# Optimization experiments

Measured on AMD Instinct MI355X. Metric: run time of the kernel, lower is better.

## Reference

```python
import jax, jax.numpy as jnp
from jax import lax
import numpy as np

EPS = 2.220446049250313e-16  # sys.float_info.epsilon


def setup_inputs() -> dict:
    key = jax.random.key(0)
    k1, k2, k3, k4 = jax.random.split(key, 4)
    C, H, W, R = 256, 256, 256, 16
    x = jax.random.normal(k1, (1, C, H, W), dtype=jnp.float32)
    w1 = jax.random.normal(k2, (R, C), dtype=jnp.float32) * 0.05   # Linear(C -> C//r), no bias
    w2 = jax.random.normal(k3, (C, R), dtype=jnp.float32) * 0.05   # Linear(C//r -> C), no bias
    conv_w = jax.random.normal(k4, (1, 2, 7, 7), dtype=jnp.float32) * 0.05  # Conv2d(2,1,7)
    return {"x": x, "w1": w1, "w2": w2, "conv_w": conv_w, "kv": 1}


def reference(x, w1, w2, conv_w, kv):
    b, c, h, w = x.shape  # b == 1 (module assumes batch 1 via squeeze(0))

    def fc(v):  # shared MLP of the channel attention
        return jnp.maximum(v @ w1.T, 0.0) @ w2.T

    y_avg = fc(x.mean(axis=(2, 3)))          # [1, C]
    y_max = fc(x.max(axis=(2, 3)))           # [1, C]
    y = jax.nn.sigmoid(y_avg + y_max)        # [1, C]

    yc = y[0]
    yc = (yc - yc.min()) / (yc.max() - yc.min() + 1e-20)  # min-max normalized gates in [0,1]

    # Batched SVD over channels replaces the per-channel Python loop.
    mats = x[0]                                            # [C, H, W]
    u, s, vh = jnp.linalg.svd(mats, full_matrices=False)   # u:[C,H,K] s:[C,K] vh:[C,K,W]
    K = s.shape[-1]
    # k = int(len(s) * kv * yc[c]); singular values are sorted descending, so
    # top-k selection == keep the first k -> mask the tail.
    k = jnp.floor(K * kv * yc).astype(jnp.int32)           # [C]
    keep = jnp.arange(K)[None, :] < k[:, None]             # [C, K]
    s_m = jnp.where(keep, s, 0.0)
    recon = jnp.einsum('chk,ck,ckw->chw', u, s_m, vh)      # low-rank reconstruction
    x2 = recon[None]                                       # [1, C, H, W]

    avg_out = x2.mean(axis=1, keepdims=True)
    max_out = x2.max(axis=1, keepdims=True)
    cat = jnp.concatenate([avg_out, max_out], axis=1)      # [1, 2, H, W]
    out = lax.conv_general_dilated(cat, conv_w, (1, 1), [(3, 3), (3, 3)],
                                   dimension_numbers=('NCHW', 'OIHW', 'NCHW'))
    out = jnp.where(out < EPS, EPS, out)
    return jax.nn.sigmoid(out)
```

## Files before the change

### kernel.cpp

```cpp
#include <hip/hip_runtime.h>


#define NCH 256
#define N 256
#define NN 65536
#define NS_MAX 22

#define OFF_K 0
#define OFF_MODE 256
#define OFF_MC 512
#define OFF_COEF 768
#define OFF_SUM 12032
#define OFF_MAXHW 77568
#define OFF_MEAND 143104
#define OFF_MAXD 143616
#define OFF_T 144128
#define OFF_ALPHA 144640
#define OFF_AQ 145152
#define OFF_BQ 276224
#define OFF_ITSW 407296
#define SMALL_FLOATS 407552

#define NSH_LDS 135168
#define F16_PANEL 33792

static const float EPSF = 2.220446049250313e-16f;

typedef unsigned short u16;
typedef _Float16 h8 __attribute__((ext_vector_type(8)));
typedef float f32x4 __attribute__((ext_vector_type(4)));

__device__ __forceinline__ float rdlane(float v, int l) {
  return __uint_as_float(__builtin_amdgcn_readlane(__float_as_uint(v), l));
}

__device__ __forceinline__ u16 f2h(float v) {
  _Float16 h = (_Float16)v;
  u16 u;
  __builtin_memcpy(&u, &h, 2);
  return u;
}
__device__ __forceinline__ float h2f(u16 u) {
  _Float16 h;
  __builtin_memcpy(&h, &u, 2);
  return (float)h;
}

__device__ __forceinline__ double block_sum1024d(double v, double* red, int tid) {
  for (int off = 32; off; off >>= 1) v += __shfl_down(v, off, 64);
  __syncthreads();
  if ((tid & 63) == 0) red[tid >> 6] = v;
  __syncthreads();
  double s = 0.0;
#pragma unroll
  for (int i = 0; i < 16; ++i) s += red[i];
  return s;
}

__global__ __launch_bounds__(256) void k_chan_stats(const float* __restrict__ x,
                                                    float* __restrict__ small) {
  int c = blockIdx.x, tid = threadIdx.x;
  const float4* xc = (const float4*)(x + (size_t)c * NN);
  double s = 0.0;
  float m = -1e30f;
  for (int i = tid; i < NN / 4; i += 256) {
    float4 v = xc[i];
    s += (double)v.x + (double)v.y + (double)v.z + (double)v.w;
    m = fmaxf(m, fmaxf(fmaxf(v.x, v.y), fmaxf(v.z, v.w)));
  }
  __shared__ double rs[4];
  __shared__ float rm[4];
  for (int off = 32; off; off >>= 1) {
    s += __shfl_down(s, off, 64);
    m = fmaxf(m, __shfl_down(m, off, 64));
  }
  if ((tid & 63) == 0) { rs[tid >> 6] = s; rm[tid >> 6] = m; }
  __syncthreads();
  if (tid == 0) {
    ((double*)(small + OFF_MEAND))[c] = (rs[0] + rs[1] + rs[2] + rs[3]) / (double)NN;
    ((double*)(small + OFF_MAXD))[c] =
        (double)fmaxf(fmaxf(rm[0], rm[1]), fmaxf(rm[2], rm[3]));
  }
}

__global__ __launch_bounds__(256) void k_attention(const float* __restrict__ w1,
                                                   const float* __restrict__ w2,
                                                   const int* __restrict__ kvp,
                                                   float* __restrict__ small) {
  int tid = threadIdx.x;
  __shared__ double ha[16], hm[16], redd[8], ymn[256], ymx[256];
  double va = ((const double*)(small + OFF_MEAND))[tid];
  double vm = ((const double*)(small + OFF_MAXD))[tid];
  for (int r = 0; r < 16; ++r) {
    double wv = (double)w1[r * 256 + tid];
    double pa = wv * va, pm = wv * vm;
    for (int off = 32; off; off >>= 1) {
      pa += __shfl_down(pa, off, 64);
      pm += __shfl_down(pm, off, 64);
    }
    if ((tid & 63) == 0) { redd[tid >> 6] = pa; redd[4 + (tid >> 6)] = pm; }
    __syncthreads();
    if (tid == 0) {
      ha[r] = fmax(redd[0] + redd[1] + redd[2] + redd[3], 0.0);
      hm[r] = fmax(redd[4] + redd[5] + redd[6] + redd[7], 0.0);
    }
    __syncthreads();
  }
  double ya = 0.0, ym = 0.0;
  for (int r = 0; r < 16; ++r) {
    double wv = (double)w2[tid * 16 + r];
    ya += ha[r] * wv;
    ym += hm[r] * wv;
  }
  double y = 1.0 / (1.0 + exp(-(ya + ym)));
  ymn[tid] = y; ymx[tid] = y;
  __syncthreads();
  for (int off = 128; off; off >>= 1) {
    if (tid < off) {
      ymn[tid] = fmin(ymn[tid], ymn[tid + off]);
      ymx[tid] = fmax(ymx[tid], ymx[tid + off]);
    }
    __syncthreads();
  }
  double yc = (y - ymn[0]) / (ymx[0] - ymn[0] + 1e-20);
  int kv = kvp[0];
  int k = (int)floor(256.0 * (double)kv * yc);
  int mode = (k <= 0) ? 0 : ((k >= 256) ? 1 : 2);
  int* ip = (int*)small;
  ip[OFF_K + tid] = k;
  ip[OFF_MODE + tid] = mode;
}

#define GEMM128_VARS                                                           \
  int tid = threadIdx.x;                                                       \
  int tx4 = (tid & 15) * 4, ty4 = (tid >> 4) * 4;                              \
  int lm = tid >> 1, lq = (tid & 1) * 2;                                       \
  int lk = tid >> 4, lc = (tid & 15) * 2;                                      \
  (void)lk; (void)lc;

#define STORE_T128(Ls, v0, v1)                                                 \
  Ls[lq * 4 + 0][lm] = v0.x; Ls[lq * 4 + 1][lm] = v0.y;                        \
  Ls[lq * 4 + 2][lm] = v0.z; Ls[lq * 4 + 3][lm] = v0.w;                        \
  Ls[lq * 4 + 4][lm] = v1.x; Ls[lq * 4 + 5][lm] = v1.y;                        \
  Ls[lq * 4 + 6][lm] = v1.z; Ls[lq * 4 + 7][lm] = v1.w;

#define GEMM128_INNER(AsM, BsM)                                                \
  _Pragma("unroll") for (int kk = 0; kk < 16; ++kk) {                          \
    float4 a0 = *(const float4*)&AsM[kk][ty4];                                 \
    float4 a1 = *(const float4*)&AsM[kk][64 + ty4];                            \
    float4 b0 = *(const float4*)&BsM[kk][tx4];                                 \
    float4 b1 = *(const float4*)&BsM[kk][64 + tx4];                            \
    float av[8] = {a0.x, a0.y, a0.z, a0.w, a1.x, a1.y, a1.z, a1.w};            \
    float bv[8] = {b0.x, b0.y, b0.z, b0.w, b1.x, b1.y, b1.z, b1.w};            \
    _Pragma("unroll") for (int rr = 0; rr < 8; ++rr)                           \
      _Pragma("unroll") for (int cc2 = 0; cc2 < 8; ++cc2)                      \
        acc[rr][cc2] += av[rr] * bv[cc2];                                      \
  }

#define WRITE_TILE_NORM(Cc)                                                    \
  _Pragma("unroll") for (int rh = 0; rh < 2; ++rh)                             \
  _Pragma("unroll") for (int rr = 0; rr < 4; ++rr) {                           \
    int rI = rh * 4 + rr;                                                      \
    float* rowp = (Cc) + (size_t)(i0 + rh * 64 + ty4 + rr) * N + j0;           \
    *(float4*)(rowp + tx4) =                                                   \
        make_float4(acc[rI][0], acc[rI][1], acc[rI][2], acc[rI][3]);           \
    *(float4*)(rowp + 64 + tx4) =                                              \
        make_float4(acc[rI][4], acc[rI][5], acc[rI][6], acc[rI][7]);           \
  }

#define WRITE_TILE_MIRROR(Cc)                                                  \
  _Pragma("unroll") for (int ch = 0; ch < 2; ++ch)                             \
  _Pragma("unroll") for (int cc2 = 0; cc2 < 4; ++cc2) {                        \
    int cI = ch * 4 + cc2;                                                     \
    float* rowp = (Cc) + (size_t)(j0 + ch * 64 + tx4 + cc2) * N + i0;          \
    *(float4*)(rowp + ty4) =                                                   \
        make_float4(acc[0][cI], acc[1][cI], acc[2][cI], acc[3][cI]);           \
    *(float4*)(rowp + 64 + ty4) =                                              \
        make_float4(acc[4][cI], acc[5][cI], acc[6][cI], acc[7][cI]);           \
  }

#define SYM_MAP                                                                \
  int bx = blockIdx.x;                                                         \
  int i0 = (bx >= 1) ? 128 : 0, j0 = (bx == 2) ? 128 : 0;

__global__ __launch_bounds__(256) void k_gram(const float* __restrict__ x,
                                              float* __restrict__ bufA, int base) {
  __shared__ float As[16][132], Bs[16][132];
  GEMM128_VARS; SYM_MAP;
  const float* A = x + (size_t)(base + blockIdx.z) * NN;
  float acc[8][8] = {};
  const float* Ap = A + (size_t)(i0 + lm) * N + lq * 4;
  const float* Bp = A + (size_t)(j0 + lm) * N + lq * 4;
  float4 va0 = *(const float4*)Ap, va1 = *(const float4*)(Ap + 4);
  float4 vb0 = *(const float4*)Bp, vb1 = *(const float4*)(Bp + 4);
  for (int kt = 0; kt < 16; ++kt) {
    __syncthreads();
    STORE_T128(As, va0, va1); STORE_T128(Bs, vb0, vb1);
    __syncthreads();
    if (kt < 15) {
      va0 = *(const float4*)(Ap + (kt + 1) * 16);
      va1 = *(const float4*)(Ap + (kt + 1) * 16 + 4);
      vb0 = *(const float4*)(Bp + (kt + 1) * 16);
      vb1 = *(const float4*)(Bp + (kt + 1) * 16 + 4);
    }
    GEMM128_INNER(As, Bs);
  }
  float* Cc = bufA + (size_t)blockIdx.z * NN;
  WRITE_TILE_NORM(Cc);
  if (bx == 1) { WRITE_TILE_MIRROR(Cc); }
}

__global__ __launch_bounds__(1024) void k_tridiag(const float* __restrict__ Gall,
                                                  float* __restrict__ small, int base) {
  extern __shared__ double dls[];
  double* redd = dls;
  double* pip = dls + 16;
  float* P = (float*)(dls + 1040);
  float* uf = P + 32896;
  float* wf = uf + 256;
  int tid = threadIdx.x, lane = tid & 63;
  int r = tid & 255, g = tid >> 8;
  int R0 = ((tid >> 6) & 3) << 6;
  int c = base + blockIdx.x;
  const int* ip = (const int*)small;
  if (ip[OFF_MODE + c] != 2) return;
  const float* G = Gall + (size_t)blockIdx.x * NN;
  double* aq = (double*)(small + OFF_AQ) + (size_t)c * 256;
  double* bq = (double*)(small + OFF_BQ) + (size_t)c * 256;
  const int triR = (r * (r + 1)) >> 1;

  for (int i = g; i < N; i += 4)
    if (r <= i) P[((i * (i + 1)) >> 1) + r] = G[i * N + r];
  __syncthreads();

  for (int j = 0; j + 2 < N; ++j) {
    if (g == 0 && r >= j + 1) uf[r] = P[triR + j];
    __syncthreads();
    float ur0 = uf[r];
    double part = (g == 0 && r >= j + 2) ? (double)ur0 * (double)ur0 : 0.0;
    double x0 = (double)uf[j + 1];
    double sigma = block_sum1024d(part, redd, tid);
    if (sigma <= 1e-40) {
      if (tid == 0) bq[j] = x0;
      __syncthreads();
      continue;
    }
    double nu = sqrt(x0 * x0 + sigma);
    double bsub = (x0 >= 0.0) ? -nu : nu;
    double beta = 1.0 / (nu * (nu + fabs(x0)));
    if (tid == j + 1) uf[tid] = (float)(x0 - bsub);
    __syncthreads();
    int cbase = (j + 1) & ~63;
    int c0 = cbase + 64 * g;
    float ureg = 0.f;
    if (c0 < N) ureg = uf[c0 + lane];
    double myp = 0.0;
    if (c0 < N) {
      int lbeg = (c0 > j + 1) ? c0 : (j + 1);
      int lend = c0 + 64;
      if (lbeg < lend) {
        double pi0 = 0.0, pi1 = 0.0, pi2 = 0.0, pi3 = 0.0;
        if (c0 + 64 <= R0) {
          int lmv = lbeg;
          for (; lmv + 3 < lend; lmv += 4) {
            float uv0 = rdlane(ureg, lmv - c0), uv1 = rdlane(ureg, lmv + 1 - c0);
            float uv2 = rdlane(ureg, lmv + 2 - c0), uv3 = rdlane(ureg, lmv + 3 - c0);
            float v0 = P[triR + lmv], v1 = P[triR + lmv + 1];
            float v2 = P[triR + lmv + 2], v3 = P[triR + lmv + 3];
            pi0 += (double)v0 * (double)uv0;
            pi1 += (double)v1 * (double)uv1;
            pi2 += (double)v2 * (double)uv2;
            pi3 += (double)v3 * (double)uv3;
          }
          for (; lmv < lend; ++lmv)
            pi0 += (double)P[triR + lmv] * (double)rdlane(ureg, lmv - c0);
        } else if (c0 >= R0 + 64) {
          int lmv = lbeg;
          int s = (lmv * (lmv + 1)) >> 1;
          for (; lmv + 3 < lend; lmv += 4) {
            int s0 = s, s1 = s0 + lmv + 1, s2 = s1 + lmv + 2, s3 = s2 + lmv + 3;
            s = s3 + lmv + 4;
            float uv0 = rdlane(ureg, lmv - c0), uv1 = rdlane(ureg, lmv + 1 - c0);
            float uv2 = rdlane(ureg, lmv + 2 - c0), uv3 = rdlane(ureg, lmv + 3 - c0);
            pi0 += (double)P[s0 + r] * (double)uv0;
            pi1 += (double)P[s1 + r] * (double)uv1;
            pi2 += (double)P[s2 + r] * (double)uv2;
            pi3 += (double)P[s3 + r] * (double)uv3;
          }
          for (; lmv < lend; ++lmv) {
            pi0 += (double)P[s + r] * (double)rdlane(ureg, lmv - c0);
            s += lmv + 1;
          }
        } else {
          int lmv = lbeg;
          int s = (lmv * (lmv + 1)) >> 1;
          for (; lmv < lend; ++lmv) {
            float uv = rdlane(ureg, lmv - c0);
            float v = P[(lmv <= r) ? (triR + lmv) : (s + r)];
            pi0 += (double)v * (double)uv;
            s += lmv + 1;
          }
        }
        myp = (pi0 + pi1) + (pi2 + pi3);
      }
    }
    pip[tid] = (r >= j + 1) ? myp : 0.0;
    __syncthreads();
    double ur = (r >= j + 1) ? (double)uf[r] : 0.0;
    double pi = 0.0;
    if (g == 0 && r >= j + 1)
      pi = (pip[r] + pip[256 + r] + pip[512 + r] + pip[768 + r]) * beta;
    double kpart = (g == 0) ? ur * pi : 0.0;
    double K = block_sum1024d(kpart, redd, tid) * beta * 0.5;
    if (g == 0) wf[r] = (float)(pi - K * ur);
    __syncthreads();
    float wreg = 0.f;
    if (c0 < N) wreg = wf[c0 + lane];
    if (c0 < N && r >= j + 1) {
      float urf = uf[r];
      float wrf = wf[r];
      int lbeg = (c0 > j + 1) ? c0 : (j + 1);
      int lend = c0 + 64;
      int lcap = (r | 63) + 1;
      if (lend > lcap) lend = lcap;
      if (c0 + 64 <= R0) {
        int lmv = lbeg;
        for (; lmv + 1 < lend; lmv += 2) {
          float uv0 = rdlane(ureg, lmv - c0), wv0 = rdlane(wreg, lmv - c0);
          float uv1 = rdlane(ureg, lmv + 1 - c0), wv1 = rdlane(wreg, lmv + 1 - c0);
          P[triR + lmv] = fmaf(-wrf, uv0, fmaf(-urf, wv0, P[triR + lmv]));
          P[triR + lmv + 1] = fmaf(-wrf, uv1, fmaf(-urf, wv1, P[triR + lmv + 1]));
        }
        if (lmv < lend) {
          float uv0 = rdlane(ureg, lmv - c0), wv0 = rdlane(wreg, lmv - c0);
          P[triR + lmv] = fmaf(-wrf, uv0, fmaf(-urf, wv0, P[triR + lmv]));
        }
      } else if (c0 == R0) {
        for (int lmv = lbeg; lmv < lend; ++lmv) {
          float uv = rdlane(ureg, lmv - c0), wv = rdlane(wreg, lmv - c0);
          if (lmv <= r)
            P[triR + lmv] = fmaf(-wrf, uv, fmaf(-urf, wv, P[triR + lmv]));
        }
      }
    }
    if (tid == 0) bq[j] = bsub;
    __syncthreads();
  }
  if (g == 0) aq[r] = (double)P[triR + r];
  if (tid == 0) bq[N - 2] = (double)P[(((N - 1) * N) >> 1) + N - 2];
}

__device__ __forceinline__ int sturm_count_lds(const double* a, const double* b,
                                               double t) {
  double d = a[0] - t;
  int cnt = (d < 0.0);
  for (int i = 1; i < N; ++i) {
    double den = d;
    if (fabs(den) < 1e-20) den = (den < 0.0) ? -1e-20 : 1e-20;
    double bb = b[i - 1];
    d = (a[i] - t) - bb * bb / den;
    cnt += (d < 0.0);
  }
  return cnt;
}

__global__ __launch_bounds__(64) void k_bisect(float* __restrict__ small,
                                               int base, int cc) {
  int ci = blockIdx.x;
  if (ci >= cc) return;
  int c = base + ci, lane = threadIdx.x;
  int* ip = (int*)small;
  if (ip[OFF_MODE + c] != 2) {
    if (lane == 0) { ip[OFF_MC + c] = 0; ip[OFF_ITSW + c] = 0; }
    return;
  }
  int k = ip[OFF_K + c];
  const double* a = (const double*)(small + OFF_AQ) + (size_t)c * 256;
  const double* b = (const double*)(small + OFF_BQ) + (size_t)c * 256;
  __shared__ double sa[256], sb[256];
  for (int i = lane; i < N; i += 64) {
    sa[i] = a[i];
    if (i < N - 1) sb[i] = b[i];
  }
  __syncthreads();
  double lo = 1e300, hi = -1e300;
  for (int i = lane; i < N; i += 64) {
    double rr = (i > 0 ? fabs(sb[i - 1]) : 0.0) + (i < N - 1 ? fabs(sb[i]) : 0.0);
    lo = fmin(lo, sa[i] - rr);
    hi = fmax(hi, sa[i] + rr);
  }
  for (int off = 32; off; off >>= 1) {
    lo = fmin(lo, __shfl_xor(lo, off, 64));
    hi = fmax(hi, __shfl_xor(hi, off, 64));
  }
  double lamk = 0.0, lamk1 = 0.0;
  for (int which = 0; which < 2; ++which) {
    int j = (which == 0) ? (N - k + 1) : (N - k);
    double l0 = lo, h0 = hi;
    for (int pass = 0; pass < 10; ++pass) {
      double step = (h0 - l0) * (1.0 / 65.0);
      double t = l0 + step * (double)(lane + 1);
      int cnt = sturm_count_lds(sa, sb, t);
      unsigned long long mask = __ballot(cnt >= j);
      if (mask == 0ull) {
        l0 = l0 + step * 64.0;
      } else {
        int bpos = __ffsll((long long)mask) - 1;
        double nl = (bpos == 0) ? l0 : (l0 + step * (double)bpos);
        h0 = l0 + step * (double)(bpos + 1);
        l0 = nl;
      }
    }
    double v = 0.5 * (l0 + h0);
    if (which == 0) lamk = v; else lamk1 = v;
  }
  if (lane == 0) {
    double t = 0.5 * (lamk + lamk1);
    double gap = fmax(lamk - lamk1, 0.0);
    double alpha = 1.002 * fmax(hi - t, t - lo) + 1e-30;
    double g0 = fmax(gap / (2.0 * alpha), 2e-6);
    float* cf = small + OFF_COEF + (size_t)c * (2 * NS_MAX);
    double l = fmin(g0, 0.99);
    int m = 0, isw = NS_MAX;
    while (m < NS_MAX - 2 && l < 0.9999) {
      if (isw == NS_MAX && l >= 0.02) isw = m;
      double aa = sqrt(27.0 / (4.0 * (1.0 + l + l * l)));
      double bb = (4.0 / 27.0) * aa * aa * aa;
      cf[2 * m] = (float)aa;
      cf[2 * m + 1] = (float)bb;
      double pl = aa * l - bb * l * l * l;
      double p1 = aa - bb;
      l = fmin(pl, p1);
      m++;
    }
    for (int e = 0; e < 2; ++e) {
      if (isw == NS_MAX && l >= 0.02) isw = m;
      cf[2 * m] = 1.5f; cf[2 * m + 1] = 0.5f; m++;
    }
    if (isw > m) isw = m;
    ip[OFF_MC + c] = m;
    ip[OFF_ITSW + c] = isw;
    ((double*)(small + OFF_T))[c] = t;
    ((double*)(small + OFF_ALPHA))[c] = alpha;
  }
}

__global__ void k_x0(const float* __restrict__ small, float* __restrict__ bufA,
                     int base) {
  int ci = blockIdx.y, c = base + ci;
  const int* ip = (const int*)small;
  if (ip[OFF_MODE + c] != 2) return;
  double t = ((const double*)(small + OFF_T))[c];
  double inva = 1.0 / ((const double*)(small + OFF_ALPHA))[c];
  float* X = bufA + (size_t)ci * NN;
  int r = blockIdx.x, tid = threadIdx.x;
  double gg = (double)X[r * N + tid];
  if (tid == r) gg -= t;
  X[r * N + tid] = (float)(gg * inva);
}

__global__ __launch_bounds__(256) void k_ns1(const float* __restrict__ src,
                                             float* __restrict__ Sb,
                                             const float* __restrict__ small,
                                             int base, int it) {
  const int* ip = (const int*)small;
  int c = base + blockIdx.z;
  if (ip[OFF_MODE + c] != 2 || it >= ip[OFF_ITSW + c]) return;
  __shared__ float As[16][132], Bs[16][132];
  GEMM128_VARS; SYM_MAP;
  const float* X = src + (size_t)blockIdx.z * NN;
  float acc[8][8] = {};
  const float* Ap = X + (size_t)(i0 + lm) * N + lq * 4;
  const float* Bp = X + (size_t)(j0 + lm) * N + lq * 4;
  float4 va0 = *(const float4*)Ap, va1 = *(const float4*)(Ap + 4);
  float4 vb0 = *(const float4*)Bp, vb1 = *(const float4*)(Bp + 4);
  for (int kt = 0; kt < 16; ++kt) {
    __syncthreads();
    STORE_T128(As, va0, va1); STORE_T128(Bs, vb0, vb1);
    __syncthreads();
    if (kt < 15) {
      va0 = *(const float4*)(Ap + (kt + 1) * 16);
      va1 = *(const float4*)(Ap + (kt + 1) * 16 + 4);
      vb0 = *(const float4*)(Bp + (kt + 1) * 16);
      vb1 = *(const float4*)(Bp + (kt + 1) * 16 + 4);
    }
    GEMM128_INNER(As, Bs);
  }
  float* Cc = Sb + (size_t)blockIdx.z * NN;
  WRITE_TILE_NORM(Cc);
  if (bx == 1) { WRITE_TILE_MIRROR(Cc); }
}

__global__ __launch_bounds__(256) void k_ns2(const float* __restrict__ src,
                                             const float* __restrict__ Sb,
                                             float* __restrict__ dst,
                                             const float* __restrict__ small,
                                             int base, int it) {
  const int* ip = (const int*)small;
  int c = base + blockIdx.z;
  if (ip[OFF_MODE + c] != 2 || it >= ip[OFF_ITSW + c]) return;
  float ca = small[OFF_COEF + (size_t)c * (2 * NS_MAX) + 2 * it];
  float cb = small[OFF_COEF + (size_t)c * (2 * NS_MAX) + 2 * it + 1];
  __shared__ float As[16][132], Bs[16][132];
  GEMM128_VARS; SYM_MAP;
  const float* X = src + (size_t)blockIdx.z * NN;
  const float* S = Sb + (size_t)blockIdx.z * NN;
  float acc[8][8] = {};
  const float* Ap = X + (size_t)(i0 + lm) * N + lq * 4;
  const float* Bp = S + (size_t)(j0 + lm) * N + lq * 4;
  float4 va0 = *(const float4*)Ap, va1 = *(const float4*)(Ap + 4);
  float4 vb0 = *(const float4*)Bp, vb1 = *(const float4*)(Bp + 4);
  for (int kt = 0; kt < 16; ++kt) {
    __syncthreads();
    STORE_T128(As, va0, va1); STORE_T128(Bs, vb0, vb1);
    __syncthreads();
    if (kt < 15) {
      va0 = *(const float4*)(Ap + (kt + 1) * 16);
      va1 = *(const float4*)(Ap + (kt + 1) * 16 + 4);
      vb0 = *(const float4*)(Bp + (kt + 1) * 16);
      vb1 = *(const float4*)(Bp + (kt + 1) * 16 + 4);
    }
    GEMM128_INNER(As, Bs);
  }
#pragma unroll
  for (int rh = 0; rh < 2; ++rh)
#pragma unroll
    for (int rr = 0; rr < 4; ++rr) {
      int rI = rh * 4 + rr;
      const float* rowp = X + (size_t)(i0 + rh * 64 + ty4 + rr) * N + j0;
      float4 x0 = *(const float4*)(rowp + tx4);
      float4 x1 = *(const float4*)(rowp + 64 + tx4);
      acc[rI][0] = ca * x0.x - cb * acc[rI][0];
      acc[rI][1] = ca * x0.y - cb * acc[rI][1];
      acc[rI][2] = ca * x0.z - cb * acc[rI][2];
      acc[rI][3] = ca * x0.w - cb * acc[rI][3];
      acc[rI][4] = ca * x1.x - cb * acc[rI][4];
      acc[rI][5] = ca * x1.y - cb * acc[rI][5];
      acc[rI][6] = ca * x1.z - cb * acc[rI][6];
      acc[rI][7] = ca * x1.w - cb * acc[rI][7];
    }
  float* Y = dst + (size_t)blockIdx.z * NN;
  WRITE_TILE_NORM(Y);
  if (bx == 1) { WRITE_TILE_MIRROR(Y); }
}

__device__ __forceinline__ void stage_h(u16* pan, const u16* g16, int tid) {
#pragma unroll
  for (int i = 0; i < 16; ++i) {
    int g = tid * 16 + i * 4096;
    int lo = g + ((g >> 9) << 4);
    *(uint4*)((char*)pan + lo) = *(const uint4*)((const char*)g16 + g);
  }
}
__device__ __forceinline__ void stage_f(u16* pan, const float* gF, int tid) {
#pragma unroll
  for (int i = 0; i < 16; ++i) {
    int e = tid * 8 + i * 2048;
    float4 v0 = *(const float4*)(gF + e);
    float4 v1 = *(const float4*)(gF + e + 4);
    h8 hv;
    hv[0] = (_Float16)v0.x; hv[1] = (_Float16)v0.y;
    hv[2] = (_Float16)v0.z; hv[3] = (_Float16)v0.w;
    hv[4] = (_Float16)v1.x; hv[5] = (_Float16)v1.y;
    hv[6] = (_Float16)v1.z; hv[7] = (_Float16)v1.w;
    int b = e * 2;
    int lo = b + ((b >> 9) << 4);
    *(h8*)((char*)pan + lo) = hv;
  }
}

__global__ __launch_bounds__(256) void k_nsh(const float* __restrict__ srcF,
                                             float* __restrict__ Sf,
                                             float* __restrict__ dstF,
                                             const float* __restrict__ small,
                                             int base, int it, int phase) {
  const int* ip = (const int*)small;
  int ci = blockIdx.z, c = base + ci;
  if (ip[OFF_MODE + c] != 2) return;
  int isw = ip[OFF_ITSW + c], mc = ip[OFF_MC + c];
  if (it < isw || it >= mc) return;
  SYM_MAP;
  extern __shared__ char ldsraw[];
  u16* Apan = (u16*)ldsraw;
  u16* Bpan = Apan + F16_PANEL;
  int tid = threadIdx.x;
  bool cvtA = (it == isw);
  bool sameP = (phase == 0) && (bx != 1);
  const float* XF = srcF + (size_t)ci * NN;
  const u16* XH = (const u16*)XF;
  if (cvtA) stage_f(Apan, XF + (size_t)i0 * N, tid);
  else      stage_h(Apan, XH + (size_t)i0 * N, tid);
  if (!sameP) {
    if (phase == 0) {
      if (cvtA) stage_f(Bpan, XF + (size_t)j0 * N, tid);
      else      stage_h(Bpan, XH + (size_t)j0 * N, tid);
    } else {
      const u16* SH = (const u16*)(Sf + (size_t)ci * NN);
      stage_h(Bpan, SH + (size_t)j0 * N, tid);
    }
  }
  const u16* Bb = sameP ? Apan : Bpan;
  __syncthreads();

  int l = tid & 63, wid = tid >> 6;
  int wr = (wid >> 1) * 64, wc = (wid & 1) * 64;
  int rA = wr + (l & 15), rB = wc + (l & 15);
  int kB = (l >> 4) << 3;
  f32x4 zero = {0.f, 0.f, 0.f, 0.f};
  f32x4 acc[4][4];
#pragma unroll
  for (int mi = 0; mi < 4; ++mi)
#pragma unroll
    for (int ni = 0; ni < 4; ++ni) acc[mi][ni] = zero;

#pragma unroll
  for (int kc = 0; kc < 8; ++kc) {
    int kof = kc * 32 + kB;
    h8 af[4], bf[4];
#pragma unroll
    for (int mi = 0; mi < 4; ++mi)
      af[mi] = *(const h8*)((const char*)Apan +
                            ((size_t)(rA + mi * 16) * 264 + kof) * 2);
#pragma unroll
    for (int ni = 0; ni < 4; ++ni)
      bf[ni] = *(const h8*)((const char*)Bb +
                            ((size_t)(rB + ni * 16) * 264 + kof) * 2);
#pragma unroll
    for (int mi = 0; mi < 4; ++mi)
#pragma unroll
      for (int ni = 0; ni < 4; ++ni)
        acc[mi][ni] = __builtin_amdgcn_mfma_f32_16x16x32_f16(
            af[mi], bf[ni], acc[mi][ni], 0, 0, 0);
  }

  float cav = 0.f, cbv = 0.f;
  bool last = false;
  if (phase) {
    cav = small[OFF_COEF + (size_t)c * (2 * NS_MAX) + 2 * it];
    cbv = small[OFF_COEF + (size_t)c * (2 * NS_MAX) + 2 * it + 1];
    last = (it == mc - 1);
  }
  float* oF = dstF + (size_t)ci * NN;
  u16* oH = phase ? (u16*)oF : (u16*)(Sf + (size_t)ci * NN);
  int lr4 = (l >> 4) << 2, lcn = l & 15;
#pragma unroll
  for (int mi = 0; mi < 4; ++mi)
#pragma unroll
    for (int ni = 0; ni < 4; ++ni)
#pragma unroll
      for (int rg = 0; rg < 4; ++rg) {
        int gr = i0 + wr + mi * 16 + lr4 + rg;
        int gc = j0 + wc + ni * 16 + lcn;
        float v = acc[mi][ni][rg];
        if (phase) {
          float xv = h2f(Apan[(size_t)(gr - i0) * 264 + gc]);
          v = cav * xv - cbv * v;
        }
        if (!last) {
          u16 hv = f2h(v);
          oH[(size_t)gr * N + gc] = hv;
          if (bx == 1) oH[(size_t)gc * N + gr] = hv;
        } else {
          oF[(size_t)gr * N + gc] = v;
          if (bx == 1) oF[(size_t)gc * N + gr] = v;
        }
      }
}

__global__ __launch_bounds__(256) void k_proj(const float* __restrict__ bufA,
                                              const float* __restrict__ bufB,
                                              const float* __restrict__ x,
                                              float* __restrict__ bufC,
                                              const float* __restrict__ small,
                                              int base) {
  const int* ip = (const int*)small;
  int ci = blockIdx.z, c = base + ci;
  int mode = ip[OFF_MODE + c];
  GEMM128_VARS;
  int i0 = blockIdx.x * 128, j0 = blockIdx.y * 128;
  float* Cc = bufC + (size_t)ci * NN;
  const float* xc = x + (size_t)c * NN;
  if (mode != 2) {
#pragma unroll
    for (int rh = 0; rh < 2; ++rh)
#pragma unroll
      for (int rr = 0; rr < 4; ++rr) {
        size_t ro = (size_t)(i0 + rh * 64 + ty4 + rr) * N + j0;
        if (mode == 0) {
          *(float4*)(Cc + ro + tx4) = make_float4(0.f, 0.f, 0.f, 0.f);
          *(float4*)(Cc + ro + 64 + tx4) = make_float4(0.f, 0.f, 0.f, 0.f);
        } else {
          *(float4*)(Cc + ro + tx4) = *(const float4*)(xc + ro + tx4);
          *(float4*)(Cc + ro + 64 + tx4) = *(const float4*)(xc + ro + 64 + tx4);
        }
      }
    return;
  }
  int mc = ip[OFF_MC + c];
  const float* Xh = ((mc & 1) ? bufB : bufA) + (size_t)ci * NN;
  __shared__ float As[16][132], Bs[16][132];
  float acc[8][8] = {};
  const float* Ap = Xh + (size_t)(i0 + lm) * N + lq * 4;
  const float* Bp = xc + (size_t)lk * N + j0 + lc * 4;
  float4 va0 = *(const float4*)Ap, va1 = *(const float4*)(Ap + 4);
  float4 vb0 = *(const float4*)Bp, vb1 = *(const float4*)(Bp + 4);
  for (int kt = 0; kt < 16; ++kt) {
    __syncthreads();
    STORE_T128(As, va0, va1);
    *(float4*)&Bs[lk][lc * 4] = vb0;
    *(float4*)&Bs[lk][(lc + 1) * 4] = vb1;
    __syncthreads();
    if (kt < 15) {
      va0 = *(const float4*)(Ap + (kt + 1) * 16);
      va1 = *(const float4*)(Ap + (kt + 1) * 16 + 4);
      const float* Bp2 = xc + (size_t)((kt + 1) * 16 + lk) * N + j0 + lc * 4;
      vb0 = *(const float4*)Bp2;
      vb1 = *(const float4*)(Bp2 + 4);
    }
    GEMM128_INNER(As, Bs);
  }
#pragma unroll
  for (int rh = 0; rh < 2; ++rh)
#pragma unroll
    for (int rr = 0; rr < 4; ++rr) {
      int rI = rh * 4 + rr;
      const float* rowp = xc + (size_t)(i0 + rh * 64 + ty4 + rr) * N + j0;
      float4 x0 = *(const float4*)(rowp + tx4);
      float4 x1 = *(const float4*)(rowp + 64 + tx4);
      acc[rI][0] = 0.5f * (acc[rI][0] + x0.x);
      acc[rI][1] = 0.5f * (acc[rI][1] + x0.y);
      acc[rI][2] = 0.5f * (acc[rI][2] + x0.z);
      acc[rI][3] = 0.5f * (acc[rI][3] + x0.w);
      acc[rI][4] = 0.5f * (acc[rI][4] + x1.x);
      acc[rI][5] = 0.5f * (acc[rI][5] + x1.y);
      acc[rI][6] = 0.5f * (acc[rI][6] + x1.z);
      acc[rI][7] = 0.5f * (acc[rI][7] + x1.w);
    }
  WRITE_TILE_NORM(Cc);
}

__global__ void k_accum(const float* __restrict__ bufC, float* __restrict__ sum_hw,
                        float* __restrict__ max_hw, int cc, int first) {
  int p = blockIdx.x * 256 + threadIdx.x;
  float s = first ? 0.f : sum_hw[p];
  float m = first ? -1e30f : max_hw[p];
  for (int ci = 0; ci < cc; ++ci) {
    float v = bufC[(size_t)ci * NN + p];
    s += v;
    m = fmaxf(m, v);
  }
  sum_hw[p] = s;
  max_hw[p] = m;
}

__global__ void k_conv(const float* __restrict__ sum_hw, const float* __restrict__ max_hw,
                       const float* __restrict__ cw, float* __restrict__ out) {
  int p = blockIdx.x * 256 + threadIdx.x;
  int h = p >> 8, w = p & 255;
  float acc = 0.f;
  for (int dy = 0; dy < 7; ++dy) {
    int hy = h + dy - 3;
    if (hy < 0 || hy > 255) continue;
    for (int dx = 0; dx < 7; ++dx) {
      int wx = w + dx - 3;
      if (wx < 0 || wx > 255) continue;
      int q = hy * 256 + wx;
      acc += cw[dy * 7 + dx] * (sum_hw[q] * (1.f / 256.f)) +
             cw[49 + dy * 7 + dx] * max_hw[q];
    }
  }
  acc = fmaxf(acc, EPSF);
  out[p] = 1.f / (1.f + expf(-acc));
}

extern "C" void kernel_launch(void* const* d_in, const int* in_sizes, int n_in,
                              void* d_out, int out_size, void* d_ws, size_t ws_size,
                              hipStream_t stream) {
  const float* x = (const float*)d_in[0];
  const float* w1 = (const float*)d_in[1];
  const float* w2 = (const float*)d_in[2];
  const float* cw = (const float*)d_in[3];
  const int* kv = (const int*)d_in[4];
  float* out = (float*)d_out;
  float* small = (float*)d_ws;

  size_t small_bytes = (size_t)SMALL_FLOATS * 4;
  size_t avail = ws_size > small_bytes ? ws_size - small_bytes : 0;
  long chunk = (long)(avail / (3ull * NN * 4));
  if (chunk > NCH) chunk = NCH;
  if (chunk < 1) chunk = 1;
  float* bufA = small + SMALL_FLOATS;
  float* bufB = bufA + (size_t)chunk * NN;
  float* bufC = bufB + (size_t)chunk * NN;

  const int tridiag_lds = 1040 * 8 + 32896 * 4 + 512 * 4;
  hipFuncSetAttribute((const void*)k_tridiag,
                      hipFuncAttributeMaxDynamicSharedMemorySize, tridiag_lds);
  hipFuncSetAttribute((const void*)k_nsh,
                      hipFuncAttributeMaxDynamicSharedMemorySize, NSH_LDS);

  k_chan_stats<<<NCH, 256, 0, stream>>>(x, small);
  k_attention<<<1, 256, 0, stream>>>(w1, w2, kv, small);

  const int IT32 = 13;

  for (int base = 0; base < NCH; base += (int)chunk) {
    int cc = (NCH - base < (int)chunk) ? (NCH - base) : (int)chunk;
    dim3 gsym(3, 1, cc);
    dim3 gproj(2, 2, cc);
    k_gram<<<gsym, 256, 0, stream>>>(x, bufA, base);
    k_tridiag<<<cc, 1024, tridiag_lds, stream>>>(bufA, small, base);
    k_bisect<<<cc, 64, 0, stream>>>(small, base, cc);
    k_x0<<<dim3(N, cc), 256, 0, stream>>>(small, bufA, base);
    for (int it = 0; it < NS_MAX; ++it) {
      const float* src = (it & 1) ? bufB : bufA;
      float* dst = (it & 1) ? bufA : bufB;
      if (it < IT32) {
        k_ns1<<<gsym, 256, 0, stream>>>(src, bufC, small, base, it);
        k_ns2<<<gsym, 256, 0, stream>>>(src, bufC, dst, small, base, it);
      }
      k_nsh<<<gsym, 256, NSH_LDS, stream>>>(src, bufC, dst, small, base, it, 0);
      k_nsh<<<gsym, 256, NSH_LDS, stream>>>(src, bufC, dst, small, base, it, 1);
    }
    k_proj<<<gproj, 256, 0, stream>>>(bufA, bufB, x, bufC, small, base);
    k_accum<<<256, 256, 0, stream>>>(bufC, small + OFF_SUM, small + OFF_MAXHW, cc,
                                     base == 0 ? 1 : 0);
  }
  k_conv<<<256, 256, 0, stream>>>(small + OFF_SUM, small + OFF_MAXHW, cw, out);
}
```

Measured before the change: 5.786 ms.

## Restructure tridiagonalization to 512 threads and fold norm and matvec into one barrier phase

The Householder tridiagonalization kernel now runs with 512 threads, so each wave handles two 64-column chunks instead of one. The sigma reduction is overlapped with the symmetric matvec: the matvec is computed with the un-modified Householder vector, and the pivot-element change is corrected afterwards with a rank-one fix term. This removes roughly two block barriers per column step and replaces the generic 16-entry block reduction with an 8-wave one. The cost is fewer threads doing the matvec and update work, and a small numerical difference from the corrected-pivot formulation.

```diff
diff --git a/kernel.cpp b/kernel.cpp
--- a/kernel.cpp
+++ b/kernel.cpp
@@ -46,17 +46,6 @@
   return (float)h;
 }
 
-__device__ __forceinline__ double block_sum1024d(double v, double* red, int tid) {
-  for (int off = 32; off; off >>= 1) v += __shfl_down(v, off, 64);
-  __syncthreads();
-  if ((tid & 63) == 0) red[tid >> 6] = v;
-  __syncthreads();
-  double s = 0.0;
-#pragma unroll
-  for (int i = 0; i < 16; ++i) s += red[i];
-  return s;
-}
-
 __global__ __launch_bounds__(256) void k_chan_stats(const float* __restrict__ x,
                                                     float* __restrict__ small) {
   int c = blockIdx.x, tid = threadIdx.x;
@@ -210,17 +199,102 @@
   if (bx == 1) { WRITE_TILE_MIRROR(Cc); }
 }
 
-__global__ __launch_bounds__(1024) void k_tridiag(const float* __restrict__ Gall,
-                                                  float* __restrict__ small, int base) {
+__device__ __forceinline__ double mv_chunk(const float* __restrict__ P, int c0,
+                                           int j, int r, int R0, int triR,
+                                           float ureg) {
+  double pi0 = 0.0, pi1 = 0.0, pi2 = 0.0, pi3 = 0.0;
+  if (c0 < N) {
+    int lbeg = (c0 > j + 1) ? c0 : (j + 1);
+    int lend = c0 + 64;
+    if (lbeg < lend) {
+      if (c0 + 64 <= R0) {
+        int lmv = lbeg;
+        for (; lmv + 3 < lend; lmv += 4) {
+          float uv0 = rdlane(ureg, lmv - c0), uv1 = rdlane(ureg, lmv + 1 - c0);
+          float uv2 = rdlane(ureg, lmv + 2 - c0), uv3 = rdlane(ureg, lmv + 3 - c0);
+          float v0 = P[triR + lmv], v1 = P[triR + lmv + 1];
+          float v2 = P[triR + lmv + 2], v3 = P[triR + lmv + 3];
+          pi0 += (double)v0 * (double)uv0;
+          pi1 += (double)v1 * (double)uv1;
+          pi2 += (double)v2 * (double)uv2;
+          pi3 += (double)v3 * (double)uv3;
+        }
+        for (; lmv < lend; ++lmv)
+          pi0 += (double)P[triR + lmv] * (double)rdlane(ureg, lmv - c0);
+      } else if (c0 >= R0 + 64) {
+        int lmv = lbeg;
+        int s = (lmv * (lmv + 1)) >> 1;
+        for (; lmv + 3 < lend; lmv += 4) {
+          int s0 = s, s1 = s0 + lmv + 1, s2 = s1 + lmv + 2, s3 = s2 + lmv + 3;
+          s = s3 + lmv + 4;
+          float uv0 = rdlane(ureg, lmv - c0), uv1 = rdlane(ureg, lmv + 1 - c0);
+          float uv2 = rdlane(ureg, lmv + 2 - c0), uv3 = rdlane(ureg, lmv + 3 - c0);
+          pi0 += (double)P[s0 + r] * (double)uv0;
+          pi1 += (double)P[s1 + r] * (double)uv1;
+          pi2 += (double)P[s2 + r] * (double)uv2;
+          pi3 += (double)P[s3 + r] * (double)uv3;
+        }
+        for (; lmv < lend; ++lmv) {
+          pi0 += (double)P[s + r] * (double)rdlane(ureg, lmv - c0);
+          s += lmv + 1;
+        }
+      } else {
+        int lmv = lbeg;
+        int s = (lmv * (lmv + 1)) >> 1;
+        for (; lmv < lend; ++lmv) {
+          float uv = rdlane(ureg, lmv - c0);
+          float v = P[(lmv <= r) ? (triR + lmv) : (s + r)];
+          pi0 += (double)v * (double)uv;
+          s += lmv + 1;
+        }
+      }
+    }
+  }
+  return (pi0 + pi1) + (pi2 + pi3);
+}
+
+__device__ __forceinline__ void upd_chunk(float* __restrict__ P, int c0, int j,
+                                          int r, int R0, int triR, float ureg,
+                                          float wreg, float urf, float wrf) {
+  if (c0 >= N) return;
+  int lbeg = (c0 > j + 1) ? c0 : (j + 1);
+  int lend = c0 + 64;
+  int lcap = (r | 63) + 1;
+  if (lend > lcap) lend = lcap;
+  if (c0 + 64 <= R0) {
+    int lmv = lbeg;
+    for (; lmv + 1 < lend; lmv += 2) {
+      float uv0 = rdlane(ureg, lmv - c0), wv0 = rdlane(wreg, lmv - c0);
+      float uv1 = rdlane(ureg, lmv + 1 - c0), wv1 = rdlane(wreg, lmv + 1 - c0);
+      P[triR + lmv] = fmaf(-wrf, uv0, fmaf(-urf, wv0, P[triR + lmv]));
+      P[triR + lmv + 1] = fmaf(-wrf, uv1, fmaf(-urf, wv1, P[triR + lmv + 1]));
+    }
+    if (lmv < lend) {
+      float uv0 = rdlane(ureg, lmv - c0), wv0 = rdlane(wreg, lmv - c0);
+      P[triR + lmv] = fmaf(-wrf, uv0, fmaf(-urf, wv0, P[triR + lmv]));
+    }
+  } else if (c0 == R0) {
+    for (int lmv = lbeg; lmv < lend; ++lmv) {
+      float uv = rdlane(ureg, lmv - c0), wv = rdlane(wreg, lmv - c0);
+      if (lmv <= r)
+        P[triR + lmv] = fmaf(-wrf, uv, fmaf(-urf, wv, P[triR + lmv]));
+    }
+  }
+}
+
+__global__ __launch_bounds__(512) void k_tridiag(const float* __restrict__ Gall,
+                                                 float* __restrict__ small, int base) {
   extern __shared__ double dls[];
   double* redd = dls;
+  double* redd2 = dls + 8;
   double* pip = dls + 16;
-  float* P = (float*)(dls + 1040);
+  float* P = (float*)(dls + 528);
   float* uf = P + 32896;
   float* wf = uf + 256;
   int tid = threadIdx.x, lane = tid & 63;
   int r = tid & 255, g = tid >> 8;
-  int R0 = ((tid >> 6) & 3) << 6;
+  int wid = tid >> 6;
+  int R0 = (wid & 3) << 6;
   int c = base + blockIdx.x;
   const int* ip = (const int*)small;
   if (ip[OFF_MODE + c] != 2) return;
@@ -229,119 +303,63 @@
   double* bq = (double*)(small + OFF_BQ) + (size_t)c * 256;
   const int triR = (r * (r + 1)) >> 1;
 
-  for (int i = g; i < N; i += 4)
+  for (int i = g; i < N; i += 2)
     if (r <= i) P[((i * (i + 1)) >> 1) + r] = G[i * N + r];
   __syncthreads();
 
   for (int j = 0; j + 2 < N; ++j) {
     if (g == 0 && r >= j + 1) uf[r] = P[triR + j];
     __syncthreads();
-    float ur0 = uf[r];
-    double part = (g == 0 && r >= j + 2) ? (double)ur0 * (double)ur0 : 0.0;
+    float x_r = uf[r];
     double x0 = (double)uf[j + 1];
-    double sigma = block_sum1024d(part, redd, tid);
+    int cbase = (j + 1) & ~63;
+    int c0a = cbase + 128 * g, c0b = c0a + 64;
+    float urega = 0.f, uregb = 0.f;
+    if (c0a < N) urega = uf[c0a + lane];
+    if (c0b < N) uregb = uf[c0b + lane];
+    double sp = (g == 0 && r >= j + 2) ? (double)x_r * (double)x_r : 0.0;
+    double myp = mv_chunk(P, c0a, j, r, R0, triR, urega) +
+                 mv_chunk(P, c0b, j, r, R0, triR, uregb);
+    pip[tid] = (r >= j + 1) ? myp : 0.0;
+    for (int off = 32; off; off >>= 1) sp += __shfl_down(sp, off, 64);
+    if (lane == 0) redd[wid] = sp;
+    __syncthreads();
+    double sigma = ((redd[0] + redd[1]) + (redd[2] + redd[3])) +
+                   ((redd[4] + redd[5]) + (redd[6] + redd[7]));
     if (sigma <= 1e-40) {
       if (tid == 0) bq[j] = x0;
-      __syncthreads();
       continue;
     }
     double nu = sqrt(x0 * x0 + sigma);
     double bsub = (x0 >= 0.0) ? -nu : nu;
     double beta = 1.0 / (nu * (nu + fabs(x0)));
-    if (tid == j + 1) uf[tid] = (float)(x0 - bsub);
-    __syncthreads();
-    int cbase = (j + 1) & ~63;
-    int c0 = cbase + 64 * g;
-    float ureg = 0.f;
-    if (c0 < N) ureg = uf[c0 + lane];
-    double myp = 0.0;
-    if (c0 < N) {
-      int lbeg = (c0 > j + 1) ? c0 : (j + 1);
-      int lend = c0 + 64;
-      if (lbeg < lend) {
-        double pi0 = 0.0, pi1 = 0.0, pi2 = 0.0, pi3 = 0.0;
-        if (c0 + 64 <= R0) {
-          int lmv = lbeg;
-          for (; lmv + 3 < lend; lmv += 4) {
-            float uv0 = rdlane(ureg, lmv - c0), uv1 = rdlane(ureg, lmv + 1 - c0);
-            float uv2 = rdlane(ureg, lmv + 2 - c0), uv3 = rdlane(ureg, lmv + 3 - c0);
-            float v0 = P[triR + lmv], v1 = P[triR + lmv + 1];
-            float v2 = P[triR + lmv + 2], v3 = P[triR + lmv + 3];
-            pi0 += (double)v0 * (double)uv0;
-            pi1 += (double)v1 * (double)uv1;
-            pi2 += (double)v2 * (double)uv2;
-            pi3 += (double)v3 * (double)uv3;
-          }
-          for (; lmv < lend; ++lmv)
-            pi0 += (double)P[triR + lmv] * (double)rdlane(ureg, lmv - c0);
-        } else if (c0 >= R0 + 64) {
-          int lmv = lbeg;
-          int s = (lmv * (lmv + 1)) >> 1;
-          for (; lmv + 3 < lend; lmv += 4) {
-            int s0 = s, s1 = s0 + lmv + 1, s2 = s1 + lmv + 2, s3 = s2 + lmv + 3;
-            s = s3 + lmv + 4;
-            float uv0 = rdlane(ureg, lmv - c0), uv1 = rdlane(ureg, lmv + 1 - c0);
-            float uv2 = rdlane(ureg, lmv + 2 - c0), uv3 = rdlane(ureg, lmv + 3 - c0);
-            pi0 += (double)P[s0 + r] * (double)uv0;
-            pi1 += (double)P[s1 + r] * (double)uv1;
-            pi2 += (double)P[s2 + r] * (double)uv2;
-            pi3 += (double)P[s3 + r] * (double)uv3;
-          }
-          for (; lmv < lend; ++lmv) {
-            pi0 += (double)P[s + r] * (double)rdlane(ureg, lmv - c0);
-            s += lmv + 1;
-          }
-        } else {
-          int lmv = lbeg;
-          int s = (lmv * (lmv + 1)) >> 1;
-          for (; lmv < lend; ++lmv) {
-            float uv = rdlane(ureg, lmv - c0);
-            float v = P[(lmv <= r) ? (triR + lmv) : (s + r)];
-            pi0 += (double)v * (double)uv;
-            s += lmv + 1;
-          }
-        }
-        myp = (pi0 + pi1) + (pi2 + pi3);
-      }
-    }
-    pip[tid] = (r >= j + 1) ? myp : 0.0;
-    __syncthreads();
-    double ur = (r >= j + 1) ? (double)uf[r] : 0.0;
-    double pi = 0.0;
-    if (g == 0 && r >= j + 1)
-      pi = (pip[r] + pip[256 + r] + pip[512 + r] + pip[768 + r]) * beta;
-    double kpart = (g == 0) ? ur * pi : 0.0;
-    double K = block_sum1024d(kpart, redd, tid) * beta * 0.5;
-    if (g == 0) wf[r] = (float)(pi - K * ur);
-    __syncthreads();
-    float wreg = 0.f;
-    if (c0 < N) wreg = wf[c0 + lane];
-    if (c0 < N && r >= j + 1) {
-      float urf = uf[r];
+    if (c0a <= j + 1 && j + 1 < c0a + 64 && lane == j + 1 - c0a)
+      urega = (float)(x0 - bsub);
+    if (c0b <= j + 1 && j + 1 < c0b + 64 && lane == j + 1 - c0b)
+      uregb = (float)(x0 - bsub);
+    double pi = 0.0, u_r = 0.0, kp = 0.0;
+    if (r >= j + 1) {
+      double fix = -bsub * (double)P[triR + (j + 1)];
+      pi = (pip[r] + pip[256 + r] + fix) * beta;
+      u_r = (r == j + 1) ? (x0 - bsub) : (double)x_r;
+      kp = u_r * pi * 0.5;
+    }
+    for (int off = 32; off; off >>= 1) kp += __shfl_down(kp, off, 64);
+    if (lane == 0) redd2[wid] = kp;
+    __syncthreads();
+    double K = (((redd2[0] + redd2[1]) + (redd2[2] + redd2[3])) +
+                ((redd2[4] + redd2[5]) + (redd2[6] + redd2[7]))) *
+               beta * 0.5;
+    if (g == 0 && r >= j + 1) wf[r] = (float)(pi - K * u_r);
+    __syncthreads();
+    float wrega = 0.f, wregb = 0.f;
+    if (c0a < N) wrega = wf[c0a + lane];
+    if (c0b < N) wregb = wf[c0b + lane];
+    if (r >= j + 1) {
+      float urf = (float)u_r;
       float wrf = wf[r];
-      int lbeg = (c0 > j + 1) ? c0 : (j + 1);
-      int lend = c0 + 64;
-      int lcap = (r | 63) + 1;
-      if (lend > lcap) lend = lcap;
-      if (c0 + 64 <= R0) {
-        int lmv = lbeg;
-        for (; lmv + 1 < lend; lmv += 2) {
-          float uv0 = rdlane(ureg, lmv - c0), wv0 = rdlane(wreg, lmv - c0);
-          float uv1 = rdlane(ureg, lmv + 1 - c0), wv1 = rdlane(wreg, lmv + 1 - c0);
-          P[triR + lmv] = fmaf(-wrf, uv0, fmaf(-urf, wv0, P[triR + lmv]));
-          P[triR + lmv + 1] = fmaf(-wrf, uv1, fmaf(-urf, wv1, P[triR + lmv + 1]));
-        }
-        if (lmv < lend) {
-          float uv0 = rdlane(ureg, lmv - c0), wv0 = rdlane(wreg, lmv - c0);
-          P[triR + lmv] = fmaf(-wrf, uv0, fmaf(-urf, wv0, P[triR + lmv]));
-        }
-      } else if (c0 == R0) {
-        for (int lmv = lbeg; lmv < lend; ++lmv) {
-          float uv = rdlane(ureg, lmv - c0), wv = rdlane(wreg, lmv - c0);
-          if (lmv <= r)
-            P[triR + lmv] = fmaf(-wrf, uv, fmaf(-urf, wv, P[triR + lmv]));
-        }
-      }
+      upd_chunk(P, c0a, j, r, R0, triR, urega, wrega, urf, wrf);
+      upd_chunk(P, c0b, j, r, R0, triR, uregb, wregb, urf, wrf);
     }
     if (tid == 0) bq[j] = bsub;
     __syncthreads();
@@ -793,7 +811,7 @@
   float* bufB = bufA + (size_t)chunk * NN;
   float* bufC = bufB + (size_t)chunk * NN;
 
-  const int tridiag_lds = 1040 * 8 + 32896 * 4 + 512 * 4;
+  const int tridiag_lds = 528 * 8 + 32896 * 4 + 512 * 4;
   hipFuncSetAttribute((const void*)k_tridiag,
                       hipFuncAttributeMaxDynamicSharedMemorySize, tridiag_lds);
   hipFuncSetAttribute((const void*)k_nsh,
@@ -809,7 +827,7 @@
     dim3 gsym(3, 1, cc);
     dim3 gproj(2, 2, cc);
     k_gram<<<gsym, 256, 0, stream>>>(x, bufA, base);
-    k_tridiag<<<cc, 1024, tridiag_lds, stream>>>(bufA, small, base);
+    k_tridiag<<<cc, 512, tridiag_lds, stream>>>(bufA, small, base);
     k_bisect<<<cc, 64, 0, stream>>>(small, base, cc);
     k_x0<<<dim3(N, cc), 256, 0, stream>>>(small, bufA, base);
     for (int it = 0; it < NS_MAX; ++it) {
```

Measured after the change: 5.757 ms. About the same (-0.5%).
